# Performance work log

Hardware: AMD Instinct MI355X
Metric: run time of the kernel (lower is better)

Reference implementation:

```python
import jax, jax.numpy as jnp
import numpy as np

N, IN_DIM, HID, E = 2048, 128, 64, 32768
EPS = 1e-5  # torch BatchNorm1d / LayerNorm default eps


def setup_inputs() -> dict:
    key = jax.random.key(0)
    ks = jax.random.split(key, 12)
    s = 0.05
    return {
        "h": jax.random.normal(ks[0], (N, IN_DIM), jnp.float32),
        "local": jax.random.normal(ks[1], (N, IN_DIM), jnp.float32),
        "e": jax.random.normal(ks[2], (E, HID), jnp.float32),
        "src": jax.random.randint(ks[3], (E,), 0, N, jnp.int32),
        "dst": jax.random.randint(ks[4], (E,), 0, N, jnp.int32),
        "ln_w": jnp.ones((IN_DIM,), jnp.float32),
        "ln_b": jnp.zeros((IN_DIM,), jnp.float32),
        "conv_w": jax.random.normal(ks[5], (1, 2, 3), jnp.float32) * 0.3,
        "conv_b": jnp.zeros((1,), jnp.float32),
        "W1": jax.random.normal(ks[6], (IN_DIM, HID * HID), jnp.float32) * s,
        "b1": jnp.zeros((HID * HID,), jnp.float32),
        "Wp2": jax.random.normal(ks[7], (IN_DIM, HID), jnp.float32) * s,
        "bp2": jnp.zeros((HID,), jnp.float32),
        "W2": jax.random.normal(ks[8], (IN_DIM, HID), jnp.float32) * s,
        "b2": jnp.zeros((HID,), jnp.float32),
        "W3": jax.random.normal(ks[9], (HID, HID), jnp.float32) * s,
        "b3": jnp.zeros((HID,), jnp.float32),
        "bng_g": jnp.ones((HID,), jnp.float32),
        "bng_b": jnp.zeros((HID,), jnp.float32),
        "bnG_g": jnp.ones((HID,), jnp.float32),
        "bnG_b": jnp.zeros((HID,), jnp.float32),
        "bnL_g": jnp.ones((HID,), jnp.float32),
        "bnL_b": jnp.zeros((HID,), jnp.float32),
    }


def _bn_eval(x, g, b):
    # BatchNorm1d in eval mode, running_mean=0, running_var=1
    return x * (g / jnp.sqrt(1.0 + EPS)) + b


def _layernorm(x, w, b):
    mu = jnp.mean(x, axis=-1, keepdims=True)
    var = jnp.var(x, axis=-1, keepdims=True)
    return (x - mu) / jnp.sqrt(var + EPS) * w + b


def reference(h, local, e, src, dst, ln_w, ln_b, conv_w, conv_b,
              W1, b1, Wp2, bp2, W2, b2, W3, b3,
              bng_g, bng_b, bnG_g, bnG_b, bnL_g, bnL_b):
    # ---- local edge branch ----
    edge = jnp.stack([local[src], local[dst]], axis=1)  # [E, 2, in_dim]
    edge = _layernorm(edge, ln_w, ln_b)
    # Conv1d(2 -> 1, k=3, pad=1) over the in_dim axis
    lr_local = jax.lax.conv_general_dilated(
        edge, conv_w, window_strides=(1,), padding=[(1, 1)],
        dimension_numbers=("NCH", "OIH", "NCH"))[:, 0, :] + conv_b  # [E, in_dim]
    lr_local = jax.nn.relu(lr_local)  # dropout is identity in eval
    lr_local = lr_local @ W2 + b2  # [E, hid]

    # ---- global edge branch ----
    p1 = jax.nn.relu(h @ W1 + b1).reshape(h.shape[0], HID, HID)  # [N, hid(d), hid(k)]
    p2 = jax.nn.relu(h @ Wp2 + bp2)  # [N, hid(k)]
    # mm[i, j, d] = sum_k p1[i, d, k] * p2[j, k]; gather only needed edges
    lr_global = jnp.einsum("edk,ek->ed", p1[src], p2[dst])  # [E, hid]
    lr_global = _bn_eval(lr_global, bng_g, bng_b) @ W3 + b3
    lr_global = jax.nn.relu(_bn_eval(lr_global, bnG_g, bnG_b))

    lr_local = jax.nn.relu(_bn_eval(lr_local, bnL_g, bnL_b))
    return lr_local + lr_global + e
```

## Files before the change

kernel.cpp:

```cpp
#include <hip/hip_runtime.h>

#define N_NODES 2048
#define IN_DIM 128
#define HID 64
#define N_EDGES 32768
#define EPS 1e-5f
#define CAP 64
#define TPN 4
#define NTILES (N_NODES * TPN)
#define POISON ((int)0xAAAAAAAA)

typedef short short8 __attribute__((ext_vector_type(8)));
typedef float f32x4 __attribute__((ext_vector_type(4)));

__device__ __forceinline__ float relu_f(float x) { return fmaxf(x, 0.f); }

__device__ __forceinline__ unsigned short f2bf(float f) {
  unsigned int u = __float_as_uint(f);
  u = (u + 0x7fffu + ((u >> 16) & 1u)) >> 16;
  return (unsigned short)u;
}
__device__ __forceinline__ float bf2f(unsigned short h) {
  return __uint_as_float(((unsigned int)h) << 16);
}
__device__ __forceinline__ short8 pack8(const float* f) {
  short8 o;
  #pragma unroll
  for (int i = 0; i < 8; ++i) o[i] = (short)f2bf(f[i]);
  return o;
}

__global__ __launch_bounds__(256) void prep_scatter(
    const float* __restrict__ h, const float* __restrict__ local,
    const float* __restrict__ ln_w, const float* __restrict__ ln_b,
    const float* __restrict__ Wp2, const float* __restrict__ bp2,
    const float* __restrict__ W1, const float* __restrict__ W2,
    const float* __restrict__ W3, const int* __restrict__ src,
    const int* __restrict__ dst,
    unsigned short* __restrict__ hb, unsigned short* __restrict__ lnlb,
    unsigned short* __restrict__ p2b, unsigned short* __restrict__ w1t,
    unsigned short* __restrict__ w2tb, unsigned short* __restrict__ w3tb,
    int* __restrict__ cursor, int2* __restrict__ slot_ed)
{
  __shared__ __align__(16) union {
    struct { float tile[IN_DIM][65]; } tr;
    struct { float hs[4][IN_DIM]; } p2s;
  } S;
  const int b = blockIdx.x, t = threadIdx.x;
  const int w = t >> 6, l = t & 63;

  if (b < 128) {
    int base = b * 2048 + t * 8;
    float4 v0 = *(const float4*)(h + base);
    float4 v1 = *(const float4*)(h + base + 4);
    ushort4 o0, o1;
    o0.x = f2bf(v0.x); o0.y = f2bf(v0.y); o0.z = f2bf(v0.z); o0.w = f2bf(v0.w);
    o1.x = f2bf(v1.x); o1.y = f2bf(v1.y); o1.z = f2bf(v1.z); o1.w = f2bf(v1.w);
    *(ushort4*)(hb + base) = o0;
    *(ushort4*)(hb + base + 4) = o1;
  } else if (b < 256) {
    int nb = b - 128;
    #pragma unroll
    for (int i = 0; i < 4; ++i) {
      int row = nb * 16 + w * 4 + i;
      const float* x = local + (size_t)row * IN_DIM;
      float x0 = x[l], x1 = x[l + 64];
      float s1 = x0 + x1, s2 = x0 * x0 + x1 * x1;
      #pragma unroll
      for (int off = 32; off > 0; off >>= 1) {
        s1 += __shfl_xor(s1, off);
        s2 += __shfl_xor(s2, off);
      }
      float mean = s1 * (1.f / IN_DIM);
      float var = s2 * (1.f / IN_DIM) - mean * mean;
      float rstd = rsqrtf(var + EPS);
      unsigned short* o = lnlb + (size_t)row * IN_DIM;
      o[l]      = f2bf((x0 - mean) * rstd * ln_w[l] + ln_b[l]);
      o[l + 64] = f2bf((x1 - mean) * rstd * ln_w[l + 64] + ln_b[l + 64]);
    }
    if (b == 128) {
      for (int i = t; i < IN_DIM * HID; i += 256) {
        int x = i >> 6, j = i & 63;
        w2tb[j * IN_DIM + x] = f2bf(W2[i]);
      }
    } else if (b == 129) {
      for (int i = t; i < HID * HID; i += 256) {
        int k = i >> 6, j = i & 63;
        w3tb[j * HID + k] = f2bf(W3[i]);
      }
    }
  } else if (b < 384) {
    int pb = b - 256;
    #pragma unroll
    for (int i = 0; i < 4; ++i) {
      int row = pb * 16 + w * 4 + i;
      S.p2s.hs[w][l] = h[(size_t)row * IN_DIM + l];
      S.p2s.hs[w][l + 64] = h[(size_t)row * IN_DIM + 64 + l];
      float acc = bp2[l];
      #pragma unroll 8
      for (int m = 0; m < IN_DIM; ++m) acc += S.p2s.hs[w][m] * Wp2[m * HID + l];
      p2b[(size_t)row * HID + l] = f2bf(relu_f(acc));
    }
  } else if (b < 448) {
    int n0 = (b - 384) * 64;
    int tx = t & 63, ty = t >> 6;
    #pragma unroll
    for (int r = 0; r < 32; ++r) {
      int k = r * 4 + ty;
      S.tr.tile[k][tx] = W1[(size_t)k * 4096 + n0 + tx];
    }
    __syncthreads();
    int j = t >> 2, kb = (t & 3) * 32;
    #pragma unroll
    for (int c = 0; c < 8; ++c) {
      ushort4 o;
      o.x = f2bf(S.tr.tile[kb + c * 4 + 0][j]);
      o.y = f2bf(S.tr.tile[kb + c * 4 + 1][j]);
      o.z = f2bf(S.tr.tile[kb + c * 4 + 2][j]);
      o.w = f2bf(S.tr.tile[kb + c * 4 + 3][j]);
      *(ushort4*)&w1t[(size_t)(n0 + j) * 128 + kb + c * 4] = o;
    }
  } else {
    int base = (b - 448) * 512;
    #pragma unroll
    for (int it = 0; it < 2; ++it) {
      int e = base + it * 256 + t;
      int s = src[e];
      int r = atomicAdd(&cursor[s], 1) - POISON;
      if (r < CAP) slot_ed[s * CAP + r] = make_int2(e, dst[e]);
    }
  }
}

__global__ __launch_bounds__(256) void p1_gemm(
    const unsigned short* __restrict__ hb, const unsigned short* __restrict__ w1t,
    const float* __restrict__ b1, unsigned short* __restrict__ p1b)
{
  const int b = blockIdx.x, t = threadIdx.x;
  const int w = t >> 6, l = t & 63;
  const int lr = l & 15, lq = l >> 4;
  const int bm = (b & 31) * 64;
  const int bn = (b >> 5) * 128;
  const int m0 = bm + w * 16;

  f32x4 acc[8];
  #pragma unroll
  for (int ni = 0; ni < 8; ++ni) acc[ni] = (f32x4){0.f, 0.f, 0.f, 0.f};
  #pragma unroll
  for (int k0 = 0; k0 < 128; k0 += 32) {
    short8 bmf = *(const short8*)(hb + (size_t)(m0 + lr) * 128 + k0 + lq * 8);
    #pragma unroll
    for (int ni = 0; ni < 8; ++ni) {
      short8 a = *(const short8*)(w1t + (size_t)(bn + ni * 16 + lr) * 128 + k0 + lq * 8);
      acc[ni] = __builtin_amdgcn_mfma_f32_16x16x32_bf16(a, bmf, acc[ni], 0, 0, 0);
    }
  }
  const int m = m0 + lr;
  #pragma unroll
  for (int ni = 0; ni < 8; ++ni) {
    int n = bn + ni * 16 + lq * 4;
    float4 bv = *(const float4*)&b1[n];
    ushort4 o;
    o.x = f2bf(relu_f(acc[ni][0] + bv.x));
    o.y = f2bf(relu_f(acc[ni][1] + bv.y));
    o.z = f2bf(relu_f(acc[ni][2] + bv.z));
    o.w = f2bf(relu_f(acc[ni][3] + bv.w));
    *(ushort4*)&p1b[(size_t)m * 4096 + n] = o;
  }
}

__global__ __launch_bounds__(256) void edge_mfma(
    const unsigned short* __restrict__ p1b, const unsigned short* __restrict__ p2b,
    const unsigned short* __restrict__ lnlb,
    const int2* __restrict__ slot_ed,
    const unsigned short* __restrict__ w2tb, const unsigned short* __restrict__ w3tb,
    const float* __restrict__ conv_w, const float* __restrict__ conv_b,
    const float* __restrict__ b2, const float* __restrict__ b3,
    const float* __restrict__ bng_g, const float* __restrict__ bng_b,
    const float* __restrict__ bnG_g, const float* __restrict__ bnG_b,
    const float* __restrict__ bnL_g, const float* __restrict__ bnL_b,
    const float* __restrict__ e_in, float* __restrict__ out)
{
  __shared__ float gs[4][16][68];

  const int t = threadIdx.x;
  const int w = t >> 6, l = t & 63;
  const int lr = l & 15, lq = l >> 4;
  const float rs = rsqrtf(1.f + EPS);

  const int tile = blockIdx.x * 4 + w;
  const int2 ed = slot_ed[tile * 16 + lr];
  const int eidx = ed.x;
  if (!__any(eidx >= 0)) return;
  const int srcn = tile >> 2;
  const int dn = (eidx >= 0) ? ed.y : 0;

  float bngG[4], bngB[4], bnGG[4], bnGB[4], b3c[4], bnLG[4], bnLB[4], b2c[4];
  #pragma unroll
  for (int ni = 0; ni < 4; ++ni) {
    int col = ni * 16 + lr;
    bngG[ni] = bng_g[col] * rs; bngB[ni] = bng_b[col];
    bnGG[ni] = bnG_g[col] * rs; bnGB[ni] = bnG_b[col];
    bnLG[ni] = bnL_g[col] * rs; bnLB[ni] = bnL_b[col];
    b3c[ni] = b3[col]; b2c[ni] = b2[col];
  }
  const float cw0 = conv_w[0], cw1 = conv_w[1], cw2 = conv_w[2];
  const float cw3 = conv_w[3], cw4 = conv_w[4], cw5 = conv_w[5];
  const float cb = conv_b[0];

  const unsigned short* rowd = lnlb + (size_t)dn * IN_DIM;
  const unsigned short* rows = lnlb + (size_t)srcn * IN_DIM;
  short8 bch[4], ach[4];
  #pragma unroll
  for (int ks = 0; ks < 4; ++ks) {
    bch[ks] = *(const short8*)(rowd + ks * 32 + lq * 8);
    ach[ks] = *(const short8*)(rows + ks * 32 + lq * 8);
  }
  float aL[4], aR[4], bL[4], bR[4];
  #pragma unroll
  for (int ks = 0; ks < 4; ++ks) {
    int kL = ks * 32 + lq * 8 - 1;
    int kR = ks * 32 + lq * 8 + 8;
    bool vL = (kL >= 0), vR = (kR < IN_DIM);
    aL[ks] = vL ? bf2f(rows[kL]) : 0.f;
    bL[ks] = vL ? bf2f(rowd[kL]) : 0.f;
    aR[ks] = vR ? bf2f(rows[kR]) : 0.f;
    bR[ks] = vR ? bf2f(rowd[kR]) : 0.f;
  }
  f32x4 v[4];
  #pragma unroll
  for (int ni = 0; ni < 4; ++ni) v[ni] = (f32x4){0.f, 0.f, 0.f, 0.f};
  #pragma unroll
  for (int ks = 0; ks < 4; ++ks) {
    float A[8], B[8];
    #pragma unroll
    for (int j = 0; j < 8; ++j) {
      A[j] = bf2f((unsigned short)ach[ks][j]);
      B[j] = bf2f((unsigned short)bch[ks][j]);
    }
    short8 af;
    #pragma unroll
    for (int j = 0; j < 8; ++j) {
      float am = j ? A[j - 1] : aL[ks];
      float ap = (j < 7) ? A[j + 1] : aR[ks];
      float bm = j ? B[j - 1] : bL[ks];
      float bp = (j < 7) ? B[j + 1] : bR[ks];
      float cv = relu_f(cw0 * am + cw1 * A[j] + cw2 * ap +
                        cw3 * bm + cw4 * B[j] + cw5 * bp + cb);
      af[j] = (short)f2bf(cv);
    }
    #pragma unroll
    for (int ni = 0; ni < 4; ++ni) {
      short8 wb = *(const short8*)(w2tb + (size_t)(ni * 16 + lr) * IN_DIM + ks * 32 + lq * 8);
      v[ni] = __builtin_amdgcn_mfma_f32_16x16x32_bf16(af, wb, v[ni], 0, 0, 0);
    }
  }

  const unsigned short* p2r = p2b + (size_t)dn * HID + lq * 8;
  short8 a0 = *(const short8*)(p2r);
  short8 a1 = *(const short8*)(p2r + 32);
  const unsigned short* pr = p1b + (size_t)srcn * 4096 + lr * 64 + lq * 8;
  f32x4 c[4];
  #pragma unroll
  for (int ni = 0; ni < 4; ++ni) {
    c[ni] = (f32x4){0.f, 0.f, 0.f, 0.f};
    short8 pb0 = *(const short8*)(pr + ni * 1024);
    short8 pb1 = *(const short8*)(pr + ni * 1024 + 32);
    c[ni] = __builtin_amdgcn_mfma_f32_16x16x32_bf16(a0, pb0, c[ni], 0, 0, 0);
    c[ni] = __builtin_amdgcn_mfma_f32_16x16x32_bf16(a1, pb1, c[ni], 0, 0, 0);
  }

  #pragma unroll
  for (int ni = 0; ni < 4; ++ni)
    #pragma unroll
    for (int r = 0; r < 4; ++r)
      gs[w][lq * 4 + r][ni * 16 + lr] = c[ni][r] * bngG[ni] + bngB[ni];
  asm volatile("s_waitcnt lgkmcnt(0)" ::: "memory");
  short8 ga0 = pack8(&gs[w][lr][lq * 8]);
  short8 ga1 = pack8(&gs[w][lr][32 + lq * 8]);

  const unsigned short* wr3 = w3tb + lr * HID + lq * 8;
  f32x4 u[4];
  #pragma unroll
  for (int ni = 0; ni < 4; ++ni) {
    u[ni] = (f32x4){0.f, 0.f, 0.f, 0.f};
    short8 wb0 = *(const short8*)(wr3 + ni * 1024);
    short8 wb1 = *(const short8*)(wr3 + ni * 1024 + 32);
    u[ni] = __builtin_amdgcn_mfma_f32_16x16x32_bf16(ga0, wb0, u[ni], 0, 0, 0);
    u[ni] = __builtin_amdgcn_mfma_f32_16x16x32_bf16(ga1, wb1, u[ni], 0, 0, 0);
  }

  int er[4];
  #pragma unroll
  for (int r = 0; r < 4; ++r) er[r] = __shfl(eidx, lq * 4 + r);
  #pragma unroll
  for (int ni = 0; ni < 4; ++ni) {
    int col = ni * 16 + lr;
    #pragma unroll
    for (int r = 0; r < 4; ++r) {
      int e = er[r];
      if (e >= 0) {
        float vg = relu_f((u[ni][r] + b3c[ni]) * bnGG[ni] + bnGB[ni]);
        float vl = relu_f((v[ni][r] + b2c[ni]) * bnLG[ni] + bnLB[ni]);
        out[(size_t)e * HID + col] = vl + vg + e_in[(size_t)e * HID + col];
      }
    }
  }
}

extern "C" void kernel_launch(void* const* d_in, const int* in_sizes, int n_in,
                              void* d_out, int out_size, void* d_ws, size_t ws_size,
                              hipStream_t stream) {
  const float* h      = (const float*)d_in[0];
  const float* local  = (const float*)d_in[1];
  const float* e_in   = (const float*)d_in[2];
  const int*   src    = (const int*)d_in[3];
  const int*   dst    = (const int*)d_in[4];
  const float* ln_w   = (const float*)d_in[5];
  const float* ln_b   = (const float*)d_in[6];
  const float* conv_w = (const float*)d_in[7];
  const float* conv_b = (const float*)d_in[8];
  const float* W1     = (const float*)d_in[9];
  const float* b1     = (const float*)d_in[10];
  const float* Wp2    = (const float*)d_in[11];
  const float* bp2    = (const float*)d_in[12];
  const float* W2     = (const float*)d_in[13];
  const float* b2     = (const float*)d_in[14];
  const float* W3     = (const float*)d_in[15];
  const float* b3     = (const float*)d_in[16];
  const float* bng_g  = (const float*)d_in[17];
  const float* bng_b  = (const float*)d_in[18];
  const float* bnG_g  = (const float*)d_in[19];
  const float* bnG_b  = (const float*)d_in[20];
  const float* bnL_g  = (const float*)d_in[21];
  const float* bnL_b  = (const float*)d_in[22];
  float* out = (float*)d_out;

  char* p = (char*)d_ws;
  unsigned short* p1b  = (unsigned short*)p; p += (size_t)N_NODES * HID * HID * 2;
  unsigned short* p2b  = (unsigned short*)p; p += (size_t)N_NODES * HID * 2;
  unsigned short* lnlb = (unsigned short*)p; p += (size_t)N_NODES * IN_DIM * 2;
  unsigned short* hb   = (unsigned short*)p; p += (size_t)N_NODES * IN_DIM * 2;
  unsigned short* w1t  = (unsigned short*)p; p += (size_t)4096 * 128 * 2;
  unsigned short* w2tb = (unsigned short*)p; p += (size_t)HID * IN_DIM * 2;
  unsigned short* w3tb = (unsigned short*)p; p += (size_t)HID * HID * 2;
  int*  cursor  = (int*)p;  p += N_NODES * 4;
  int2* slot_ed = (int2*)p; p += (size_t)NTILES * 16 * 8;


  prep_scatter<<<512, 256, 0, stream>>>(h, local, ln_w, ln_b, Wp2, bp2, W1, W2, W3,
                                        src, dst, hb, lnlb, p2b, w1t, w2tb, w3tb,
                                        cursor, slot_ed);
  p1_gemm<<<1024, 256, 0, stream>>>(hb, w1t, b1, p1b);
  edge_mfma<<<2048, 256, 0, stream>>>(p1b, p2b, lnlb, slot_ed,
                                      w2tb, w3tb, conv_w, conv_b, b2, b3,
                                      bng_g, bng_b, bnG_g, bnG_b, bnL_g, bnL_b, e_in, out);
}
```

Baseline: 175.1 us.

## Fuse W1 GEMM into prep kernel reading fp32 directly, reorder edge kernel loads

Drops the separate p1 GEMM launch and the bf16 pre-conversion and transpose of h and W1. The GEMM blocks now read fp32 h and W1 straight from global memory and convert in registers, and they run in the same launch as the layernorm, p2, weight-transpose and scatter blocks. In the edge kernel, the global-branch MFMA is moved ahead of the local conv path, source-row loads are issued before the early-exit check, per-column BN constants are loaded near their use, and launch bounds ask for 6 blocks per CU. The risk is that W1 loads become strided scalar fp32 reads repeated across 32 M-blocks, which could be slower than the old vector bf16 loads. The GEMM also no longer waits for a dependency barrier, but it did not need one.

```diff
diff --git a/kernel.cpp b/kernel.cpp
--- a/kernel.cpp
+++ b/kernel.cpp
@@ -30,39 +30,71 @@
   return o;
 }
 
-__global__ __launch_bounds__(256) void prep_scatter(
+__global__ __launch_bounds__(256) void gemm_prep(
     const float* __restrict__ h, const float* __restrict__ local,
     const float* __restrict__ ln_w, const float* __restrict__ ln_b,
     const float* __restrict__ Wp2, const float* __restrict__ bp2,
-    const float* __restrict__ W1, const float* __restrict__ W2,
-    const float* __restrict__ W3, const int* __restrict__ src,
-    const int* __restrict__ dst,
-    unsigned short* __restrict__ hb, unsigned short* __restrict__ lnlb,
-    unsigned short* __restrict__ p2b, unsigned short* __restrict__ w1t,
+    const float* __restrict__ W1, const float* __restrict__ b1,
+    const float* __restrict__ W2, const float* __restrict__ W3,
+    const int* __restrict__ src, const int* __restrict__ dst,
+    unsigned short* __restrict__ p1b, unsigned short* __restrict__ lnlb,
+    unsigned short* __restrict__ p2b,
     unsigned short* __restrict__ w2tb, unsigned short* __restrict__ w3tb,
     int* __restrict__ cursor, int2* __restrict__ slot_ed)
 {
-  __shared__ __align__(16) union {
-    struct { float tile[IN_DIM][65]; } tr;
-    struct { float hs[4][IN_DIM]; } p2s;
-  } S;
+  __shared__ __align__(16) struct { float hs[4][IN_DIM]; } S;
   const int b = blockIdx.x, t = threadIdx.x;
   const int w = t >> 6, l = t & 63;
-
-  if (b < 128) {
-    int base = b * 2048 + t * 8;
-    float4 v0 = *(const float4*)(h + base);
-    float4 v1 = *(const float4*)(h + base + 4);
-    ushort4 o0, o1;
-    o0.x = f2bf(v0.x); o0.y = f2bf(v0.y); o0.z = f2bf(v0.z); o0.w = f2bf(v0.w);
-    o1.x = f2bf(v1.x); o1.y = f2bf(v1.y); o1.z = f2bf(v1.z); o1.w = f2bf(v1.w);
-    *(ushort4*)(hb + base) = o0;
-    *(ushort4*)(hb + base + 4) = o1;
-  } else if (b < 256) {
-    int nb = b - 128;
+  const int lr = l & 15, lq = l >> 4;
+
+  if (b < 1024) {
+    const int bm = (b & 31) * 64;
+    const int bn = (b >> 5) * 128;
+    const int m0 = bm + w * 16;
+    f32x4 acc[8];
+    #pragma unroll
+    for (int ni = 0; ni < 8; ++ni) acc[ni] = (f32x4){0.f, 0.f, 0.f, 0.f};
+
+    #pragma unroll
+    for (int k0 = 0; k0 < 128; k0 += 32) {
+      const float* hrow = h + (size_t)(m0 + lr) * 128 + k0 + lq * 8;
+      float4 h0 = *(const float4*)hrow;
+      float4 h1 = *(const float4*)(hrow + 4);
+      short8 bmf;
+      bmf[0] = (short)f2bf(h0.x); bmf[1] = (short)f2bf(h0.y);
+      bmf[2] = (short)f2bf(h0.z); bmf[3] = (short)f2bf(h0.w);
+      bmf[4] = (short)f2bf(h1.x); bmf[5] = (short)f2bf(h1.y);
+      bmf[6] = (short)f2bf(h1.z); bmf[7] = (short)f2bf(h1.w);
+      const float* wcol = W1 + (size_t)(k0 + lq * 8) * 4096 + bn + lr;
+      #pragma unroll
+      for (int ni = 0; ni < 8; ++ni) {
+        short8 a;
+        #pragma unroll
+        for (int j = 0; j < 8; ++j)
+          a[j] = (short)f2bf(wcol[(size_t)j * 4096 + ni * 16]);
+        acc[ni] = __builtin_amdgcn_mfma_f32_16x16x32_bf16(a, bmf, acc[ni], 0, 0, 0);
+      }
+    }
+    const int m = m0 + lr;
+    #pragma unroll
+    for (int ni = 0; ni < 8; ++ni) {
+      int n = bn + ni * 16 + lq * 4;
+      float4 bv = *(const float4*)&b1[n];
+      ushort4 o;
+      o.x = f2bf(relu_f(acc[ni][0] + bv.x));
+      o.y = f2bf(relu_f(acc[ni][1] + bv.y));
+      o.z = f2bf(relu_f(acc[ni][2] + bv.z));
+      o.w = f2bf(relu_f(acc[ni][3] + bv.w));
+      *(ushort4*)&p1b[(size_t)m * 4096 + n] = o;
+    }
+    return;
+  }
+
+  const int pb = b - 1024;
+  if (pb < 128) {
     #pragma unroll
     for (int i = 0; i < 4; ++i) {
-      int row = nb * 16 + w * 4 + i;
+      int row = pb * 16 + w * 4 + i;
       const float* x = local + (size_t)row * IN_DIM;
       float x0 = x[l], x1 = x[l + 64];
       float s1 = x0 + x1, s2 = x0 * x0 + x1 * x1;
@@ -78,50 +110,30 @@
       o[l]      = f2bf((x0 - mean) * rstd * ln_w[l] + ln_b[l]);
       o[l + 64] = f2bf((x1 - mean) * rstd * ln_w[l + 64] + ln_b[l + 64]);
     }
-    if (b == 128) {
-      for (int i = t; i < IN_DIM * HID; i += 256) {
-        int x = i >> 6, j = i & 63;
-        w2tb[j * IN_DIM + x] = f2bf(W2[i]);
-      }
-    } else if (b == 129) {
-      for (int i = t; i < HID * HID; i += 256) {
-        int k = i >> 6, j = i & 63;
-        w3tb[j * HID + k] = f2bf(W3[i]);
-      }
-    }
-  } else if (b < 384) {
-    int pb = b - 256;
+  } else if (pb < 256) {
+    int qb = pb - 128;
     #pragma unroll
     for (int i = 0; i < 4; ++i) {
-      int row = pb * 16 + w * 4 + i;
-      S.p2s.hs[w][l] = h[(size_t)row * IN_DIM + l];
-      S.p2s.hs[w][l + 64] = h[(size_t)row * IN_DIM + 64 + l];
+      int row = qb * 16 + w * 4 + i;
+      S.hs[w][l] = h[(size_t)row * IN_DIM + l];
+      S.hs[w][l + 64] = h[(size_t)row * IN_DIM + 64 + l];
       float acc = bp2[l];
       #pragma unroll 8
-      for (int m = 0; m < IN_DIM; ++m) acc += S.p2s.hs[w][m] * Wp2[m * HID + l];
+      for (int m = 0; m < IN_DIM; ++m) acc += S.hs[w][m] * Wp2[m * HID + l];
       p2b[(size_t)row * HID + l] = f2bf(relu_f(acc));
     }
-  } else if (b < 448) {
-    int n0 = (b - 384) * 64;
-    int tx = t & 63, ty = t >> 6;
-    #pragma unroll
-    for (int r = 0; r < 32; ++r) {
-      int k = r * 4 + ty;
-      S.tr.tile[k][tx] = W1[(size_t)k * 4096 + n0 + tx];
-    }
-    __syncthreads();
-    int j = t >> 2, kb = (t & 3) * 32;
-    #pragma unroll
-    for (int c = 0; c < 8; ++c) {
-      ushort4 o;
-      o.x = f2bf(S.tr.tile[kb + c * 4 + 0][j]);
-      o.y = f2bf(S.tr.tile[kb + c * 4 + 1][j]);
-      o.z = f2bf(S.tr.tile[kb + c * 4 + 2][j]);
-      o.w = f2bf(S.tr.tile[kb + c * 4 + 3][j]);
-      *(ushort4*)&w1t[(size_t)(n0 + j) * 128 + kb + c * 4] = o;
+  } else if (pb == 256) {
+    for (int i = t; i < IN_DIM * HID; i += 256) {
+      int x = i >> 6, j = i & 63;
+      w2tb[j * IN_DIM + x] = f2bf(W2[i]);
+    }
+  } else if (pb == 257) {
+    for (int i = t; i < HID * HID; i += 256) {
+      int k = i >> 6, j = i & 63;
+      w3tb[j * HID + k] = f2bf(W3[i]);
     }
   } else {
-    int base = (b - 448) * 512;
+    int base = (pb - 258) * 512;
     #pragma unroll
     for (int it = 0; it < 2; ++it) {
       int e = base + it * 256 + t;
@@ -132,44 +144,7 @@
   }
 }
 
-__global__ __launch_bounds__(256) void p1_gemm(
-    const unsigned short* __restrict__ hb, const unsigned short* __restrict__ w1t,
-    const float* __restrict__ b1, unsigned short* __restrict__ p1b)
-{
-  const int b = blockIdx.x, t = threadIdx.x;
-  const int w = t >> 6, l = t & 63;
-  const int lr = l & 15, lq = l >> 4;
-  const int bm = (b & 31) * 64;
-  const int bn = (b >> 5) * 128;
-  const int m0 = bm + w * 16;
-
-  f32x4 acc[8];
-  #pragma unroll
-  for (int ni = 0; ni < 8; ++ni) acc[ni] = (f32x4){0.f, 0.f, 0.f, 0.f};
-  #pragma unroll
-  for (int k0 = 0; k0 < 128; k0 += 32) {
-    short8 bmf = *(const short8*)(hb + (size_t)(m0 + lr) * 128 + k0 + lq * 8);
-    #pragma unroll
-    for (int ni = 0; ni < 8; ++ni) {
-      short8 a = *(const short8*)(w1t + (size_t)(bn + ni * 16 + lr) * 128 + k0 + lq * 8);
-      acc[ni] = __builtin_amdgcn_mfma_f32_16x16x32_bf16(a, bmf, acc[ni], 0, 0, 0);
-    }
-  }
-  const int m = m0 + lr;
-  #pragma unroll
-  for (int ni = 0; ni < 8; ++ni) {
-    int n = bn + ni * 16 + lq * 4;
-    float4 bv = *(const float4*)&b1[n];
-    ushort4 o;
-    o.x = f2bf(relu_f(acc[ni][0] + bv.x));
-    o.y = f2bf(relu_f(acc[ni][1] + bv.y));
-    o.z = f2bf(relu_f(acc[ni][2] + bv.z));
-    o.w = f2bf(relu_f(acc[ni][3] + bv.w));
-    *(ushort4*)&p1b[(size_t)m * 4096 + n] = o;
-  }
-}
-
-__global__ __launch_bounds__(256) void edge_mfma(
+__global__ __launch_bounds__(256, 6) void edge_mfma(
     const unsigned short* __restrict__ p1b, const unsigned short* __restrict__ p2b,
     const unsigned short* __restrict__ lnlb,
     const int2* __restrict__ slot_ed,
@@ -189,33 +164,52 @@
   const float rs = rsqrtf(1.f + EPS);
 
   const int tile = blockIdx.x * 4 + w;
+  const int srcn = tile >> 2;
+
   const int2 ed = slot_ed[tile * 16 + lr];
+
+  const unsigned short* rows = lnlb + (size_t)srcn * IN_DIM;
+  short8 ach[4];
+  #pragma unroll
+  for (int ks = 0; ks < 4; ++ks)
+    ach[ks] = *(const short8*)(rows + ks * 32 + lq * 8);
+  const unsigned short* pr = p1b + (size_t)srcn * 4096 + lr * 64 + lq * 8;
+
+  if (!__any(ed.x >= 0)) return;
   const int eidx = ed.x;
-  if (!__any(eidx >= 0)) return;
-  const int srcn = tile >> 2;
   const int dn = (eidx >= 0) ? ed.y : 0;
 
-  float bngG[4], bngB[4], bnGG[4], bnGB[4], b3c[4], bnLG[4], bnLB[4], b2c[4];
+  const unsigned short* rowd = lnlb + (size_t)dn * IN_DIM;
+  short8 bch[4];
+  #pragma unroll
+  for (int ks = 0; ks < 4; ++ks)
+    bch[ks] = *(const short8*)(rowd + ks * 32 + lq * 8);
+  const unsigned short* p2r = p2b + (size_t)dn * HID + lq * 8;
+  short8 a0 = *(const short8*)(p2r);
+  short8 a1 = *(const short8*)(p2r + 32);
+
+  f32x4 c[4];
+  #pragma unroll
+  for (int ni = 0; ni < 4; ++ni) {
+    c[ni] = (f32x4){0.f, 0.f, 0.f, 0.f};
+    short8 pb0 = *(const short8*)(pr + ni * 1024);
+    short8 pb1 = *(const short8*)(pr + ni * 1024 + 32);
+    c[ni] = __builtin_amdgcn_mfma_f32_16x16x32_bf16(a0, pb0, c[ni], 0, 0, 0);
+    c[ni] = __builtin_amdgcn_mfma_f32_16x16x32_bf16(a1, pb1, c[ni], 0, 0, 0);
+  }
+
   #pragma unroll
   for (int ni = 0; ni < 4; ++ni) {
     int col = ni * 16 + lr;
-    bngG[ni] = bng_g[col] * rs; bngB[ni] = bng_b[col];
-    bnGG[ni] = bnG_g[col] * rs; bnGB[ni] = bnG_b[col];
-    bnLG[ni] = bnL_g[col] * rs; bnLB[ni] = bnL_b[col];
-    b3c[ni] = b3[col]; b2c[ni] = b2[col];
-  }
+    float g = bng_g[col] * rs, bb = bng_b[col];
+    #pragma unroll
+    for (int r = 0; r < 4; ++r)
+      gs[w][lq * 4 + r][ni * 16 + lr] = c[ni][r] * g + bb;
+  }
+
   const float cw0 = conv_w[0], cw1 = conv_w[1], cw2 = conv_w[2];
   const float cw3 = conv_w[3], cw4 = conv_w[4], cw5 = conv_w[5];
   const float cb = conv_b[0];
-
-  const unsigned short* rowd = lnlb + (size_t)dn * IN_DIM;
-  const unsigned short* rows = lnlb + (size_t)srcn * IN_DIM;
-  short8 bch[4], ach[4];
-  #pragma unroll
-  for (int ks = 0; ks < 4; ++ks) {
-    bch[ks] = *(const short8*)(rowd + ks * 32 + lq * 8);
-    ach[ks] = *(const short8*)(rows + ks * 32 + lq * 8);
-  }
   float aL[4], aR[4], bL[4], bR[4];
   #pragma unroll
   for (int ks = 0; ks < 4; ++ks) {
@@ -256,25 +250,6 @@
     }
   }
 
-  const unsigned short* p2r = p2b + (size_t)dn * HID + lq * 8;
-  short8 a0 = *(const short8*)(p2r);
-  short8 a1 = *(const short8*)(p2r + 32);
-  const unsigned short* pr = p1b + (size_t)srcn * 4096 + lr * 64 + lq * 8;
-  f32x4 c[4];
-  #pragma unroll
-  for (int ni = 0; ni < 4; ++ni) {
-    c[ni] = (f32x4){0.f, 0.f, 0.f, 0.f};
-    short8 pb0 = *(const short8*)(pr + ni * 1024);
-    short8 pb1 = *(const short8*)(pr + ni * 1024 + 32);
-    c[ni] = __builtin_amdgcn_mfma_f32_16x16x32_bf16(a0, pb0, c[ni], 0, 0, 0);
-    c[ni] = __builtin_amdgcn_mfma_f32_16x16x32_bf16(a1, pb1, c[ni], 0, 0, 0);
-  }
-
-  #pragma unroll
-  for (int ni = 0; ni < 4; ++ni)
-    #pragma unroll
-    for (int r = 0; r < 4; ++r)
-      gs[w][lq * 4 + r][ni * 16 + lr] = c[ni][r] * bngG[ni] + bngB[ni];
   asm volatile("s_waitcnt lgkmcnt(0)" ::: "memory");
   short8 ga0 = pack8(&gs[w][lr][lq * 8]);
   short8 ga1 = pack8(&gs[w][lr][32 + lq * 8]);
@@ -296,12 +271,15 @@
   #pragma unroll
   for (int ni = 0; ni < 4; ++ni) {
     int col = ni * 16 + lr;
+    float gG = bnG_g[col] * rs, bG = bnG_b[col];
+    float gL = bnL_g[col] * rs, bbL = bnL_b[col];
+    float c3 = b3[col], c2 = b2[col];
     #pragma unroll
     for (int r = 0; r < 4; ++r) {
       int e = er[r];
       if (e >= 0) {
-        float vg = relu_f((u[ni][r] + b3c[ni]) * bnGG[ni] + bnGB[ni]);
-        float vl = relu_f((v[ni][r] + b2c[ni]) * bnLG[ni] + bnLB[ni]);
+        float vg = relu_f((u[ni][r] + c3) * gG + bG);
+        float vl = relu_f((v[ni][r] + c2) * gL + bbL);
         out[(size_t)e * HID + col] = vl + vg + e_in[(size_t)e * HID + col];
       }
     }
@@ -340,18 +318,15 @@
   unsigned short* p1b  = (unsigned short*)p; p += (size_t)N_NODES * HID * HID * 2;
   unsigned short* p2b  = (unsigned short*)p; p += (size_t)N_NODES * HID * 2;
   unsigned short* lnlb = (unsigned short*)p; p += (size_t)N_NODES * IN_DIM * 2;
-  unsigned short* hb   = (unsigned short*)p; p += (size_t)N_NODES * IN_DIM * 2;
-  unsigned short* w1t  = (unsigned short*)p; p += (size_t)4096 * 128 * 2;
   unsigned short* w2tb = (unsigned short*)p; p += (size_t)HID * IN_DIM * 2;
   unsigned short* w3tb = (unsigned short*)p; p += (size_t)HID * HID * 2;
   int*  cursor  = (int*)p;  p += N_NODES * 4;
   int2* slot_ed = (int2*)p; p += (size_t)NTILES * 16 * 8;
 
 
-  prep_scatter<<<512, 256, 0, stream>>>(h, local, ln_w, ln_b, Wp2, bp2, W1, W2, W3,
-                                        src, dst, hb, lnlb, p2b, w1t, w2tb, w3tb,
-                                        cursor, slot_ed);
-  p1_gemm<<<1024, 256, 0, stream>>>(hb, w1t, b1, p1b);
+  gemm_prep<<<1346, 256, 0, stream>>>(h, local, ln_w, ln_b, Wp2, bp2, W1, b1, W2, W3,
+                                      src, dst, p1b, lnlb, p2b, w2tb, w3tb,
+                                      cursor, slot_ed);
   edge_mfma<<<2048, 256, 0, stream>>>(p1b, p2b, lnlb, slot_ed,
                                       w2tb, w3tb, conv_w, conv_b, b2, b3,
                                       bng_g, bng_b, bnG_g, bnG_b, bnL_g, bnL_b, e_in, out);
```

New measurement: 164.1 us. 1.07x faster.
